# Optimization experiments

Measured on AMD Instinct MI355X. Metric: run time of the kernel, lower is better.

The kernel has to match this reference:

```python
import jax, jax.numpy as jnp
import numpy as np

V, D, H, B, T = 32000, 256, 512, 32, 64


def setup_inputs() -> dict:
    key = jax.random.key(0)
    ks = jax.random.split(key, 8)
    return {
        "word_indices": jax.random.randint(ks[0], (B, T), 0, V),
        "num_words": jax.random.randint(ks[1], (B,), 1, T + 1),
        "encoder_state": jax.random.normal(ks[2], (B, H), jnp.float32),
        # learned params
        "embW": jax.random.uniform(ks[3], (V, D), jnp.float32, -1.0, 1.0),
        "Wg": jax.random.normal(ks[4], (D + H, 2 * H), jnp.float32) * 0.05,  # reset+update gates
        "bg": jnp.ones((2 * H,), jnp.float32),  # TF GRUCell gate bias init = 1.0
        "Wc": jax.random.normal(ks[5], (D + H, H), jnp.float32) * 0.05,      # candidate
        "bc": jnp.zeros((H,), jnp.float32),
        "Wout": jax.random.normal(ks[6], (H, V), jnp.float32) * 0.05,        # Dense(V)
        "bout": jnp.zeros((V,), jnp.float32),
    }


def reference(word_indices, num_words, encoder_state, embW, Wg, bg, Wc, bc, Wout, bout):
    # Embedding lookup: [B, T, D] -> time-major [T, B, D]
    xs = jnp.swapaxes(embW[word_indices], 0, 1)
    # sequence-length mask like tf.nn.static_rnn: [T, B, 1]
    mask = (jnp.arange(T)[:, None] < num_words[None, :])[..., None].astype(xs.dtype)

    def step(h, inp):
        x_t, m_t = inp  # [B, D], [B, 1]
        xh = jnp.concatenate([x_t, h], axis=-1)          # [B, D+H]
        r, u = jnp.split(jax.nn.sigmoid(xh @ Wg + bg), 2, axis=-1)
        c = jnp.tanh(jnp.concatenate([x_t, r * h], axis=-1) @ Wc + bc)
        h_new = u * h + (1.0 - u) * c
        out = h_new * m_t                                 # zero outputs past seq length
        h_next = m_t * h_new + (1.0 - m_t) * h            # carry state past seq length
        return h_next, out

    _, outs = jax.lax.scan(step, encoder_state, (xs, mask))  # outs: [T, B, H]
    logits = jnp.einsum('tbh,hv->btv', outs, Wout) + bout    # [B, T, V]
    return logits
```

## Files before the change

kernel.cpp:

```cpp
#include <hip/hip_runtime.h>
#include <hip/hip_bf16.h>

#define V_ 32000
#define D_ 256
#define H_ 512
#define B_ 32
#define T_ 64
#define NSL 8

typedef __attribute__((ext_vector_type(8))) __bf16 bf16x8;
typedef __attribute__((ext_vector_type(4))) float f32x4;
typedef _Float16 f16x2 __attribute__((ext_vector_type(2)));
typedef unsigned int u32t;
typedef unsigned short u16t;
typedef unsigned long long u64t;

__device__ __forceinline__ u32t pack_h16(float a, float b) {
  union { _Float16 h; unsigned short u; } lo, hi;
  lo.h = (_Float16)a; hi.h = (_Float16)b;
  return (u32t)lo.u | ((u32t)hi.u << 16);
}

__device__ __forceinline__ float f16u_to_f(u16t u) {
  union { _Float16 h; unsigned short u; } x;
  x.u = u;
  return (float)x.h;
}

__device__ __forceinline__ float dot2(u32t w, u32t h, float acc) {
#if __has_builtin(__builtin_amdgcn_fdot2)
  return __builtin_amdgcn_fdot2(__builtin_bit_cast(f16x2, w),
                                __builtin_bit_cast(f16x2, h), acc, false);
#else
  f16x2 a = __builtin_bit_cast(f16x2, w);
  f16x2 b = __builtin_bit_cast(f16x2, h);
  return acc + (float)a.x * (float)b.x + (float)a.y * (float)b.y;
#endif
}

__device__ __forceinline__ void gld_lds16(const void* g, void* l) {
  __builtin_amdgcn_global_load_lds((const __attribute__((address_space(1))) void*)g,
                                   (__attribute__((address_space(3))) void*)l,
                                   16, 0, 0);
}

__device__ __forceinline__ u32t ld_rlx(const u32t* p) {
  return __hip_atomic_load(p, __ATOMIC_RELAXED, __HIP_MEMORY_SCOPE_AGENT);
}
__device__ __forceinline__ void st_rlx(u32t* p, u32t v) {
  __hip_atomic_store(p, v, __ATOMIC_RELAXED, __HIP_MEMORY_SCOPE_AGENT);
}

__global__ __launch_bounds__(256) void k_transpose(const float* __restrict__ Wout,
                                                   __hip_bfloat16* __restrict__ WoutT) {
  __shared__ float tile[64][65];
  int v0 = blockIdx.x * 64;
  int h0 = blockIdx.y * 64;
  int tid = threadIdx.x;
#pragma unroll
  for (int i = 0; i < 16; ++i) {
    int idx = i * 256 + tid;
    int r = idx >> 6;
    int c = idx & 63;
    tile[r][c] = Wout[(size_t)(h0 + r) * V_ + v0 + c];
  }
  __syncthreads();
#pragma unroll
  for (int i = 0; i < 16; ++i) {
    int idx = i * 256 + tid;
    int rv = idx >> 6;
    int ch = idx & 63;
    WoutT[(size_t)(v0 + rv) * H_ + h0 + ch] = __float2bfloat16(tile[ch][rv]);
  }
}

__global__ __launch_bounds__(256) void k_pack_g2(const float* __restrict__ Wg,
                                                 uint4* __restrict__ Wg2) {
  int gid = blockIdx.x * 256 + threadIdx.x;
  int ks = gid & 3;
  int cq = (gid >> 2) & 127;
  int it = (gid >> 9) & 15;
  int s = gid >> 13;
  int j = (cq < 64) ? (s * 64 + cq) : (512 + s * 64 + (cq - 64));
  int k0 = ks * 128 + it * 8;
  uint4 v;
  v.x = pack_h16(Wg[(size_t)(256 + k0 + 0) * 1024 + j], Wg[(size_t)(256 + k0 + 1) * 1024 + j]);
  v.y = pack_h16(Wg[(size_t)(256 + k0 + 2) * 1024 + j], Wg[(size_t)(256 + k0 + 3) * 1024 + j]);
  v.z = pack_h16(Wg[(size_t)(256 + k0 + 4) * 1024 + j], Wg[(size_t)(256 + k0 + 5) * 1024 + j]);
  v.w = pack_h16(Wg[(size_t)(256 + k0 + 6) * 1024 + j], Wg[(size_t)(256 + k0 + 7) * 1024 + j]);
  Wg2[gid] = v;
}
__global__ __launch_bounds__(256) void k_pack_c2(const float* __restrict__ Wc,
                                                 uint4* __restrict__ Wc2) {
  int gid = blockIdx.x * 256 + threadIdx.x;
  int ks8 = gid & 7;
  int cq2 = (gid >> 3) & 63;
  int it = (gid >> 9) & 7;
  int s = gid >> 12;
  int jc = s * 64 + cq2;
  int k0 = ks8 * 64 + it * 8;
  uint4 v;
  v.x = pack_h16(Wc[(size_t)(256 + k0 + 0) * 512 + jc], Wc[(size_t)(256 + k0 + 1) * 512 + jc]);
  v.y = pack_h16(Wc[(size_t)(256 + k0 + 2) * 512 + jc], Wc[(size_t)(256 + k0 + 3) * 512 + jc]);
  v.z = pack_h16(Wc[(size_t)(256 + k0 + 4) * 512 + jc], Wc[(size_t)(256 + k0 + 5) * 512 + jc]);
  v.w = pack_h16(Wc[(size_t)(256 + k0 + 6) * 512 + jc], Wc[(size_t)(256 + k0 + 7) * 512 + jc]);
  Wc2[gid] = v;
}

__global__ __launch_bounds__(256) void k_precompute_g(const int* __restrict__ widx,
                                                      const float* __restrict__ embW,
                                                      const float* __restrict__ Wg,
                                                      const float* __restrict__ bg,
                                                      float* __restrict__ pre_g) {
  __shared__ __align__(16) float x2[D_][8];
  __shared__ int wid[8];
  int tid = threadIdx.x;
  int n0 = blockIdx.x * 8;
  if (tid < 8) wid[tid] = widx[n0 + tid];
  __syncthreads();
#pragma unroll
  for (int i = 0; i < 8; ++i)
    x2[tid][i] = embW[(size_t)wid[i] * D_ + tid];
  __syncthreads();

  int J = blockIdx.y * 256 + tid;
  float bias = bg[J];
  float acc[8];
#pragma unroll
  for (int i = 0; i < 8; ++i) acc[i] = bias;
  for (int d = 0; d < D_; ++d) {
    float4 xa = *(const float4*)&x2[d][0];
    float4 xb = *(const float4*)&x2[d][4];
    float w = Wg[(size_t)d * 1024 + J];
    acc[0] = fmaf(xa.x, w, acc[0]); acc[1] = fmaf(xa.y, w, acc[1]);
    acc[2] = fmaf(xa.z, w, acc[2]); acc[3] = fmaf(xa.w, w, acc[3]);
    acc[4] = fmaf(xb.x, w, acc[4]); acc[5] = fmaf(xb.y, w, acc[5]);
    acc[6] = fmaf(xb.z, w, acc[6]); acc[7] = fmaf(xb.w, w, acc[7]);
  }
#pragma unroll
  for (int i = 0; i < 8; ++i)
    pre_g[(size_t)(n0 + i) * 1024 + J] = acc[i];
}

__global__ __launch_bounds__(256) void k_precompute_c(const int* __restrict__ widx,
                                                      const float* __restrict__ embW,
                                                      const float* __restrict__ Wc,
                                                      const float* __restrict__ bc,
                                                      float* __restrict__ pre_c) {
  __shared__ __align__(16) float x2[D_][8];
  __shared__ int wid[8];
  int tid = threadIdx.x;
  int n0 = blockIdx.x * 8;
  if (tid < 8) wid[tid] = widx[n0 + tid];
  __syncthreads();
#pragma unroll
  for (int i = 0; i < 8; ++i)
    x2[tid][i] = embW[(size_t)wid[i] * D_ + tid];
  __syncthreads();

  int Jc = blockIdx.y * 256 + tid;
  float bias = bc[Jc];
  float acc[8];
#pragma unroll
  for (int i = 0; i < 8; ++i) acc[i] = bias;
  for (int d = 0; d < D_; ++d) {
    float4 xa = *(const float4*)&x2[d][0];
    float4 xb = *(const float4*)&x2[d][4];
    float w = Wc[(size_t)d * 512 + Jc];
    acc[0] = fmaf(xa.x, w, acc[0]); acc[1] = fmaf(xa.y, w, acc[1]);
    acc[2] = fmaf(xa.z, w, acc[2]); acc[3] = fmaf(xa.w, w, acc[3]);
    acc[4] = fmaf(xb.x, w, acc[4]); acc[5] = fmaf(xb.y, w, acc[5]);
    acc[6] = fmaf(xb.z, w, acc[6]); acc[7] = fmaf(xb.w, w, acc[7]);
  }
#pragma unroll
  for (int i = 0; i < 8; ++i)
    pre_c[(size_t)(n0 + i) * 512 + Jc] = acc[i];
}

__global__ __launch_bounds__(256) void k_gru_init(const float* __restrict__ enc,
                                                  u32t* __restrict__ HBT,
                                                  u32t* __restrict__ RHT) {
  int gid = blockIdx.x * 256 + threadIdx.x;
  int b = gid >> 9, k = gid & 511;
  u32t hv = pack_h16(enc[b * H_ + k], 0.f) & 0xffffu;
  st_rlx(&HBT[gid], hv);
  st_rlx(&RHT[gid], 0xFFFF0000u);
}

__global__ __launch_bounds__(512, 2) void k_gru7(const int* __restrict__ num_words,
                                                 const uint4* __restrict__ Wg2,
                                                 const uint4* __restrict__ Wc2,
                                                 const float* __restrict__ pre_g,
                                                 const float* __restrict__ pre_c,
                                                 u32t* __restrict__ RHT,
                                                 u32t* __restrict__ HBT,
                                                 u32t* __restrict__ A32) {
  __shared__ __align__(16) u32t h2_l[256];
  __shared__ __align__(16) u32t rh2_l[256];
  __shared__ float u_l[64];
  int bid = blockIdx.x;
  int b = bid & 31;
  int s = bid >> 5;
  int tid = threadIdx.x;
  int nw = num_words[b];

  int cq = tid >> 2, ks = tid & 3;
  int j1 = (cq < 64) ? (s * 64 + cq) : (512 + s * 64 + (cq - 64));
  int cq2 = tid >> 3, ks8 = tid & 7;
  int jc = s * 64 + cq2;

  uint4 wg[16];
#pragma unroll
  for (int i = 0; i < 16; ++i) {
    int ii = (i + ks) & 15;
    wg[i] = Wg2[(((size_t)s * 16 + ii) * 128 + cq) * 4 + ks];
  }
  uint4 wc[8];
#pragma unroll
  for (int i = 0; i < 8; ++i) {
    int ii = (i + ks8) & 7;
    wc[i] = Wc2[(((size_t)s * 8 + ii) * 64 + cq2) * 8 + ks8];
  }

  u32t* HBp = HBT + (size_t)b * 512;
  u32t* RHp = RHT + (size_t)b * 512;
  bool pub1 = (ks == 0) && (cq < 64);
  bool ulane = (ks == 0) && (cq >= 64);
  bool pub2 = (ks8 == 0);
  bool writer2 = pub2 && ((cq2 & 1) == 0);

  for (int t = 0; t < T_; ++t) {
    float pg = pre_g[((size_t)b * T_ + t) * 1024 + j1];
    float pc = pre_c[((size_t)b * T_ + t) * 512 + jc];

    __syncthreads();
    {
      u32t want = (u32t)t << 16;
      u32t v;
      do { v = ld_rlx(&HBp[tid]); } while ((v & 0xffff0000u) != want);
      ((volatile u16t*)h2_l)[tid] = (u16t)v;
    }
    __syncthreads();

    float a = 0.f;
    const uint4* h4 = (const uint4*)h2_l;
#pragma unroll
    for (int i = 0; i < 16; ++i) {
      int ii = (i + ks) & 15;
      uint4 hv = h4[ks * 16 + ii];
      a = dot2(wg[i].x, hv.x, a);
      a = dot2(wg[i].y, hv.y, a);
      a = dot2(wg[i].z, hv.z, a);
      a = dot2(wg[i].w, hv.w, a);
    }
    a += __shfl_xor(a, 1);
    a += __shfl_xor(a, 2);
    float gate = 1.f / (1.f + __expf(-(a + pg)));
    if (cq < 64) {
      float hh = f16u_to_f(((const u16t*)h2_l)[s * 64 + cq]);
      if (pub1)
        st_rlx(&RHp[s * 64 + cq],
               (pack_h16(gate * hh, 0.f) & 0xffffu) | ((u32t)(t + 1) << 16));
    } else if (ulane) {
      u_l[cq - 64] = gate;
    }

    {
      u32t want = (u32t)(t + 1) << 16;
      u32t v;
      do { v = ld_rlx(&RHp[tid]); } while ((v & 0xffff0000u) != want);
      ((volatile u16t*)rh2_l)[tid] = (u16t)v;
    }
    __syncthreads();

    float a2 = 0.f;
    const uint4* r4 = (const uint4*)rh2_l;
#pragma unroll
    for (int i = 0; i < 8; ++i) {
      int ii = (i + ks8) & 7;
      uint4 rv = r4[ks8 * 8 + ii];
      a2 = dot2(wc[i].x, rv.x, a2);
      a2 = dot2(wc[i].y, rv.y, a2);
      a2 = dot2(wc[i].z, rv.z, a2);
      a2 = dot2(wc[i].w, rv.w, a2);
    }
    a2 += __shfl_xor(a2, 1);
    a2 += __shfl_xor(a2, 2);
    a2 += __shfl_xor(a2, 4);
    float cv = tanhf(a2 + pc);
    float uu = u_l[cq2];
    float hold = f16u_to_f(((const u16t*)h2_l)[jc]);
    float hn = uu * hold + (1.f - uu) * cv;
    bool live = t < nw;
    float hnext = live ? hn : hold;
    if (pub2)
      st_rlx(&HBp[s * 64 + cq2],
             (pack_h16(hnext, 0.f) & 0xffffu) | ((u32t)(t + 1) << 16));
    u32t ma = (u32t)__hip_bfloat16_raw(__float2bfloat16(live ? hn : 0.f)).x;
    u32t oa = (u32t)__shfl_xor((int)ma, 8);
    if (writer2)
      A32[(((size_t)b * T_ + t) * 512 + jc) >> 1] = ma | (oa << 16);
  }
}

__global__ __launch_bounds__(256) void k_proj(const __hip_bfloat16* __restrict__ Ap,
                                              const __hip_bfloat16* __restrict__ BTp,
                                              const float* __restrict__ bout,
                                              float* __restrict__ C) {
  __shared__ char As[128 * 64 * 2];
  __shared__ char Bs[128 * 64 * 2];
  int tid = threadIdx.x;
  int lane = tid & 63;
  int wave = tid >> 6;
  int m0 = blockIdx.x * 128;
  int n0 = blockIdx.y * 128;
  int wm = wave >> 1, wn = wave & 1;
  f32x4 acc[4][4] = {};

  const char* Ab = (const char*)Ap;
  const char* Bb = (const char*)BTp;

  for (int ks = 0; ks < 8; ++ks) {
    int k0 = ks * 64;
    __syncthreads();
#pragma unroll
    for (int inst = 0; inst < 4; ++inst) {
      int o = inst * 4096 + wave * 1024;
      int ol = o + lane * 16;
      int r = ol >> 7;
      int cb = ol & 127;
      gld_lds16(Ab + ((size_t)(m0 + r) * 512 + k0) * 2 + cb, As + o);
      gld_lds16(Bb + ((size_t)(n0 + r) * 512 + k0) * 2 + cb, Bs + o);
    }
    __syncthreads();
#pragma unroll
    for (int kk = 0; kk < 64; kk += 32) {
      bf16x8 af[4], bfr[4];
      int cbyte = kk * 2 + ((lane >> 4) << 4);
#pragma unroll
      for (int mi = 0; mi < 4; ++mi) {
        int row = wm * 64 + mi * 16 + (lane & 15);
        af[mi] = *(const bf16x8*)(As + row * 128 + cbyte);
      }
#pragma unroll
      for (int ni = 0; ni < 4; ++ni) {
        int row = wn * 64 + ni * 16 + (lane & 15);
        bfr[ni] = *(const bf16x8*)(Bs + row * 128 + cbyte);
      }
#pragma unroll
      for (int mi = 0; mi < 4; ++mi)
#pragma unroll
        for (int ni = 0; ni < 4; ++ni)
          acc[mi][ni] = __builtin_amdgcn_mfma_f32_16x16x32_bf16(af[mi], bfr[ni], acc[mi][ni], 0, 0, 0);
    }
  }
#pragma unroll
  for (int ni = 0; ni < 4; ++ni) {
    int col = n0 + wn * 64 + ni * 16 + (lane & 15);
    float bb = bout[col];
#pragma unroll
    for (int mi = 0; mi < 4; ++mi) {
      int rbase = m0 + wm * 64 + mi * 16 + ((lane >> 4) << 2);
#pragma unroll
      for (int rr = 0; rr < 4; ++rr) {
        C[(size_t)(rbase + rr) * V_ + col] = acc[mi][ni][rr] + bb;
      }
    }
  }
}

extern "C" void kernel_launch(void* const* d_in, const int* in_sizes, int n_in,
                              void* d_out, int out_size, void* d_ws, size_t ws_size,
                              hipStream_t stream) {
  const int* widx = (const int*)d_in[0];
  const int* num_words = (const int*)d_in[1];
  const float* enc = (const float*)d_in[2];
  const float* embW = (const float*)d_in[3];
  const float* Wg = (const float*)d_in[4];
  const float* bg = (const float*)d_in[5];
  const float* Wc = (const float*)d_in[6];
  const float* bc = (const float*)d_in[7];
  const float* Wout = (const float*)d_in[8];
  const float* bout = (const float*)d_in[9];
  float* out = (float*)d_out;

  char* ws = (char*)d_ws;
  float* pre_g = (float*)(ws);
  float* pre_c = (float*)(ws + 8388608);
  __hip_bfloat16* A = (__hip_bfloat16*)(ws + 12582912);
  __hip_bfloat16* WoutT = (__hip_bfloat16*)(ws + 14680064);
  uint4* Wg2 = (uint4*)(ws + 47448064);
  uint4* Wc2 = (uint4*)(ws + 48496640);
  u32t* RHT = (u32t*)(ws + 49020928);
  u32t* HBT = (u32t*)(ws + 49086464);

  hipLaunchKernelGGL(k_pack_g2, dim3(256), dim3(256), 0, stream, Wg, Wg2);
  hipLaunchKernelGGL(k_pack_c2, dim3(128), dim3(256), 0, stream, Wc, Wc2);
  hipLaunchKernelGGL(k_transpose, dim3(500, 8), dim3(256), 0, stream, Wout, WoutT);
  hipLaunchKernelGGL(k_precompute_g, dim3(256, 4), dim3(256), 0, stream,
                     widx, embW, Wg, bg, pre_g);
  hipLaunchKernelGGL(k_precompute_c, dim3(256, 2), dim3(256), 0, stream,
                     widx, embW, Wc, bc, pre_c);
  hipLaunchKernelGGL(k_gru_init, dim3(64), dim3(256), 0, stream, enc, HBT, RHT);
  hipLaunchKernelGGL(k_gru7, dim3(32 * NSL), dim3(512), 0, stream,
                     num_words, Wg2, Wc2, pre_g, pre_c, RHT, HBT, (u32t*)A);
  hipLaunchKernelGGL(k_proj, dim3(16, 250), dim3(256), 0, stream, A, WoutT, bout, out);
}
```

Baseline: 390.5 us.

## Fuse GRU recurrence and output projection into one persistent kernel with flag-based streaming

Merges the GRU recurrence kernel and the vocabulary projection GEMM into a single 512-block launch. Blocks 0-255 run the recurrence and publish each hidden-state output with a per-timestep tag. The remaining 256 blocks spin on those tags and start 128-row projection tiles as soon as their timesteps finish, so the large GEMM overlaps the serial recurrence. It also stores pre_c in bf16 and adds an LDS XOR swizzle. The risks are spin-wait traffic, co-residency assumptions for forward progress, a wider tagged A buffer, and smaller M tiles (2x4 MFMA per wave) that reuse B less.

```diff
diff --git a/kernel.cpp b/kernel.cpp
--- a/kernel.cpp
+++ b/kernel.cpp
@@ -146,7 +146,7 @@
                                                       const float* __restrict__ embW,
                                                       const float* __restrict__ Wc,
                                                       const float* __restrict__ bc,
-                                                      float* __restrict__ pre_c) {
+                                                      __hip_bfloat16* __restrict__ pre_c) {
   __shared__ __align__(16) float x2[D_][8];
   __shared__ int wid[8];
   int tid = threadIdx.x;
@@ -174,196 +174,241 @@
   }
 #pragma unroll
   for (int i = 0; i < 8; ++i)
-    pre_c[(size_t)(n0 + i) * 512 + Jc] = acc[i];
+    pre_c[(size_t)(n0 + i) * 512 + Jc] = __float2bfloat16(acc[i]);
 }
 
 __global__ __launch_bounds__(256) void k_gru_init(const float* __restrict__ enc,
                                                   u32t* __restrict__ HBT,
-                                                  u32t* __restrict__ RHT) {
+                                                  u32t* __restrict__ RHT,
+                                                  uint4* __restrict__ AT4) {
   int gid = blockIdx.x * 256 + threadIdx.x;
   int b = gid >> 9, k = gid & 511;
   u32t hv = pack_h16(enc[b * H_ + k], 0.f) & 0xffffu;
   st_rlx(&HBT[gid], hv);
   st_rlx(&RHT[gid], 0xFFFF0000u);
-}
-
-__global__ __launch_bounds__(512, 2) void k_gru7(const int* __restrict__ num_words,
-                                                 const uint4* __restrict__ Wg2,
-                                                 const uint4* __restrict__ Wc2,
-                                                 const float* __restrict__ pre_g,
-                                                 const float* __restrict__ pre_c,
-                                                 u32t* __restrict__ RHT,
-                                                 u32t* __restrict__ HBT,
-                                                 u32t* __restrict__ A32) {
+  uint4 z = {0u, 0u, 0u, 0u};
+#pragma unroll
+  for (int i = 0; i < 16; ++i)
+    AT4[(size_t)gid * 16 + i] = z;
+}
+
+__global__ __launch_bounds__(512, 4) void k_fused(const int* __restrict__ num_words,
+                                                  const uint4* __restrict__ Wg2,
+                                                  const uint4* __restrict__ Wc2,
+                                                  const float* __restrict__ pre_g,
+                                                  const __hip_bfloat16* __restrict__ pre_c,
+                                                  u32t* __restrict__ RHT,
+                                                  u32t* __restrict__ HBT,
+                                                  u32t* __restrict__ AT,
+                                                  const __hip_bfloat16* __restrict__ BT,
+                                                  const float* __restrict__ bout,
+                                                  float* __restrict__ C) {
   __shared__ __align__(16) u32t h2_l[256];
   __shared__ __align__(16) u32t rh2_l[256];
   __shared__ float u_l[64];
+  __shared__ __align__(16) char As[128 * 128];
+  __shared__ __align__(16) char Bs[128 * 128];
   int bid = blockIdx.x;
-  int b = bid & 31;
-  int s = bid >> 5;
   int tid = threadIdx.x;
-  int nw = num_words[b];
-
-  int cq = tid >> 2, ks = tid & 3;
-  int j1 = (cq < 64) ? (s * 64 + cq) : (512 + s * 64 + (cq - 64));
-  int cq2 = tid >> 3, ks8 = tid & 7;
-  int jc = s * 64 + cq2;
-
-  uint4 wg[16];
-#pragma unroll
-  for (int i = 0; i < 16; ++i) {
-    int ii = (i + ks) & 15;
-    wg[i] = Wg2[(((size_t)s * 16 + ii) * 128 + cq) * 4 + ks];
-  }
-  uint4 wc[8];
-#pragma unroll
-  for (int i = 0; i < 8; ++i) {
-    int ii = (i + ks8) & 7;
-    wc[i] = Wc2[(((size_t)s * 8 + ii) * 64 + cq2) * 8 + ks8];
-  }
-
-  u32t* HBp = HBT + (size_t)b * 512;
-  u32t* RHp = RHT + (size_t)b * 512;
-  bool pub1 = (ks == 0) && (cq < 64);
-  bool ulane = (ks == 0) && (cq >= 64);
-  bool pub2 = (ks8 == 0);
-  bool writer2 = pub2 && ((cq2 & 1) == 0);
-
-  for (int t = 0; t < T_; ++t) {
-    float pg = pre_g[((size_t)b * T_ + t) * 1024 + j1];
-    float pc = pre_c[((size_t)b * T_ + t) * 512 + jc];
-
-    __syncthreads();
-    {
-      u32t want = (u32t)t << 16;
-      u32t v;
-      do { v = ld_rlx(&HBp[tid]); } while ((v & 0xffff0000u) != want);
-      ((volatile u16t*)h2_l)[tid] = (u16t)v;
-    }
-    __syncthreads();
-
-    float a = 0.f;
-    const uint4* h4 = (const uint4*)h2_l;
+
+  if (bid < 256) {
+    int b = bid & 31;
+    int s = bid >> 5;
+    int nw = num_words[b];
+
+    int cq = tid >> 2, ks = tid & 3;
+    int j1 = (cq < 64) ? (s * 64 + cq) : (512 + s * 64 + (cq - 64));
+    int cq2 = tid >> 3, ks8 = tid & 7;
+    int jc = s * 64 + cq2;
+
+    uint4 wg[16];
 #pragma unroll
     for (int i = 0; i < 16; ++i) {
       int ii = (i + ks) & 15;
-      uint4 hv = h4[ks * 16 + ii];
-      a = dot2(wg[i].x, hv.x, a);
-      a = dot2(wg[i].y, hv.y, a);
-      a = dot2(wg[i].z, hv.z, a);
-      a = dot2(wg[i].w, hv.w, a);
+      wg[i] = Wg2[(((size_t)s * 16 + ii) * 128 + cq) * 4 + ks];
     }
-    a += __shfl_xor(a, 1);
-    a += __shfl_xor(a, 2);
-    float gate = 1.f / (1.f + __expf(-(a + pg)));
-    if (cq < 64) {
-      float hh = f16u_to_f(((const u16t*)h2_l)[s * 64 + cq]);
-      if (pub1)
-        st_rlx(&RHp[s * 64 + cq],
-               (pack_h16(gate * hh, 0.f) & 0xffffu) | ((u32t)(t + 1) << 16));
-    } else if (ulane) {
-      u_l[cq - 64] = gate;
-    }
-
-    {
-      u32t want = (u32t)(t + 1) << 16;
-      u32t v;
-      do { v = ld_rlx(&RHp[tid]); } while ((v & 0xffff0000u) != want);
-      ((volatile u16t*)rh2_l)[tid] = (u16t)v;
-    }
-    __syncthreads();
-
-    float a2 = 0.f;
-    const uint4* r4 = (const uint4*)rh2_l;
+    uint4 wc[8];
 #pragma unroll
     for (int i = 0; i < 8; ++i) {
       int ii = (i + ks8) & 7;
-      uint4 rv = r4[ks8 * 8 + ii];
-      a2 = dot2(wc[i].x, rv.x, a2);
-      a2 = dot2(wc[i].y, rv.y, a2);
-      a2 = dot2(wc[i].z, rv.z, a2);
-      a2 = dot2(wc[i].w, rv.w, a2);
+      wc[i] = Wc2[(((size_t)s * 8 + ii) * 64 + cq2) * 8 + ks8];
     }
-    a2 += __shfl_xor(a2, 1);
-    a2 += __shfl_xor(a2, 2);
-    a2 += __shfl_xor(a2, 4);
-    float cv = tanhf(a2 + pc);
-    float uu = u_l[cq2];
-    float hold = f16u_to_f(((const u16t*)h2_l)[jc]);
-    float hn = uu * hold + (1.f - uu) * cv;
-    bool live = t < nw;
-    float hnext = live ? hn : hold;
-    if (pub2)
-      st_rlx(&HBp[s * 64 + cq2],
-             (pack_h16(hnext, 0.f) & 0xffffu) | ((u32t)(t + 1) << 16));
-    u32t ma = (u32t)__hip_bfloat16_raw(__float2bfloat16(live ? hn : 0.f)).x;
-    u32t oa = (u32t)__shfl_xor((int)ma, 8);
-    if (writer2)
-      A32[(((size_t)b * T_ + t) * 512 + jc) >> 1] = ma | (oa << 16);
-  }
-}
-
-__global__ __launch_bounds__(256) void k_proj(const __hip_bfloat16* __restrict__ Ap,
-                                              const __hip_bfloat16* __restrict__ BTp,
-                                              const float* __restrict__ bout,
-                                              float* __restrict__ C) {
-  __shared__ char As[128 * 64 * 2];
-  __shared__ char Bs[128 * 64 * 2];
-  int tid = threadIdx.x;
-  int lane = tid & 63;
-  int wave = tid >> 6;
-  int m0 = blockIdx.x * 128;
-  int n0 = blockIdx.y * 128;
-  int wm = wave >> 1, wn = wave & 1;
-  f32x4 acc[4][4] = {};
-
-  const char* Ab = (const char*)Ap;
-  const char* Bb = (const char*)BTp;
-
-  for (int ks = 0; ks < 8; ++ks) {
-    int k0 = ks * 64;
-    __syncthreads();
-#pragma unroll
-    for (int inst = 0; inst < 4; ++inst) {
-      int o = inst * 4096 + wave * 1024;
-      int ol = o + lane * 16;
-      int r = ol >> 7;
-      int cb = ol & 127;
-      gld_lds16(Ab + ((size_t)(m0 + r) * 512 + k0) * 2 + cb, As + o);
-      gld_lds16(Bb + ((size_t)(n0 + r) * 512 + k0) * 2 + cb, Bs + o);
+
+    u32t* HBp = HBT + (size_t)b * 512;
+    u32t* RHp = RHT + (size_t)b * 512;
+    bool pub1 = (ks == 0) && (cq < 64);
+    bool ulane = (ks == 0) && (cq >= 64);
+    bool pub2 = (ks8 == 0);
+
+    for (int t = 0; t < T_; ++t) {
+      float pg = pre_g[((size_t)b * T_ + t) * 1024 + j1];
+      float pc = __bfloat162float(pre_c[((size_t)b * T_ + t) * 512 + jc]);
+
+      __syncthreads();
+      {
+        u32t want = (u32t)t << 16;
+        u32t v;
+        do { v = ld_rlx(&HBp[tid]); } while ((v & 0xffff0000u) != want);
+        ((volatile u16t*)h2_l)[tid] = (u16t)v;
+      }
+      __syncthreads();
+
+      float a = 0.f;
+      const uint4* h4 = (const uint4*)h2_l;
+#pragma unroll
+      for (int i = 0; i < 16; ++i) {
+        int ii = (i + ks) & 15;
+        uint4 hv = h4[ks * 16 + ii];
+        a = dot2(wg[i].x, hv.x, a);
+        a = dot2(wg[i].y, hv.y, a);
+        a = dot2(wg[i].z, hv.z, a);
+        a = dot2(wg[i].w, hv.w, a);
+      }
+      a += __shfl_xor(a, 1);
+      a += __shfl_xor(a, 2);
+      float gate = 1.f / (1.f + __expf(-(a + pg)));
+      if (cq < 64) {
+        float hh = f16u_to_f(((const u16t*)h2_l)[s * 64 + cq]);
+        if (pub1)
+          st_rlx(&RHp[s * 64 + cq],
+                 (pack_h16(gate * hh, 0.f) & 0xffffu) | ((u32t)(t + 1) << 16));
+      } else if (ulane) {
+        u_l[cq - 64] = gate;
+      }
+
+      {
+        u32t want = (u32t)(t + 1) << 16;
+        u32t v;
+        do { v = ld_rlx(&RHp[tid]); } while ((v & 0xffff0000u) != want);
+        ((volatile u16t*)rh2_l)[tid] = (u16t)v;
+      }
+      __syncthreads();
+
+      float a2 = 0.f;
+      const uint4* r4 = (const uint4*)rh2_l;
+#pragma unroll
+      for (int i = 0; i < 8; ++i) {
+        int ii = (i + ks8) & 7;
+        uint4 rv = r4[ks8 * 8 + ii];
+        a2 = dot2(wc[i].x, rv.x, a2);
+        a2 = dot2(wc[i].y, rv.y, a2);
+        a2 = dot2(wc[i].z, rv.z, a2);
+        a2 = dot2(wc[i].w, rv.w, a2);
+      }
+      a2 += __shfl_xor(a2, 1);
+      a2 += __shfl_xor(a2, 2);
+      a2 += __shfl_xor(a2, 4);
+      float cv = tanhf(a2 + pc);
+      float uu = u_l[cq2];
+      float hold = f16u_to_f(((const u16t*)h2_l)[jc]);
+      float hn = uu * hold + (1.f - uu) * cv;
+      bool live = t < nw;
+      float hnext = live ? hn : hold;
+      if (pub2) {
+        st_rlx(&HBp[s * 64 + cq2],
+               (pack_h16(hnext, 0.f) & 0xffffu) | ((u32t)(t + 1) << 16));
+        u32t av = (u32t)__hip_bfloat16_raw(__float2bfloat16(live ? hn : 0.f)).x;
+        st_rlx(&AT[((size_t)(t * 32 + b)) * 512 + jc], av | ((u32t)(t + 1) << 16));
+      }
     }
-    __syncthreads();
-#pragma unroll
-    for (int kk = 0; kk < 64; kk += 32) {
-      bf16x8 af[4], bfr[4];
-      int cbyte = kk * 2 + ((lane >> 4) << 4);
-#pragma unroll
-      for (int mi = 0; mi < 4; ++mi) {
-        int row = wm * 64 + mi * 16 + (lane & 15);
-        af[mi] = *(const bf16x8*)(As + row * 128 + cbyte);
-      }
-#pragma unroll
-      for (int ni = 0; ni < 4; ++ni) {
-        int row = wn * 64 + ni * 16 + (lane & 15);
-        bfr[ni] = *(const bf16x8*)(Bs + row * 128 + cbyte);
-      }
-#pragma unroll
-      for (int mi = 0; mi < 4; ++mi)
-#pragma unroll
-        for (int ni = 0; ni < 4; ++ni)
-          acc[mi][ni] = __builtin_amdgcn_mfma_f32_16x16x32_bf16(af[mi], bfr[ni], acc[mi][ni], 0, 0, 0);
-    }
-  }
-#pragma unroll
-  for (int ni = 0; ni < 4; ++ni) {
-    int col = n0 + wn * 64 + ni * 16 + (lane & 15);
-    float bb = bout[col];
-#pragma unroll
-    for (int mi = 0; mi < 4; ++mi) {
-      int rbase = m0 + wm * 64 + mi * 16 + ((lane >> 4) << 2);
-#pragma unroll
-      for (int rr = 0; rr < 4; ++rr) {
-        C[(size_t)(rbase + rr) * V_ + col] = acc[mi][ni][rr] + bb;
+  } else {
+    int vid = bid - 256;
+    int lane = tid & 63;
+    int wave = tid >> 6;
+    int wm = wave >> 1;
+    int wn = wave & 1;
+    int arow = tid >> 2;
+    int akq = (tid & 3) << 4;
+    int aswz = (arow & 7) << 4;
+    const char* Bb = (const char*)BT;
+
+    for (int g4 = 0; g4 < 4; ++g4) {
+#pragma unroll 1
+      for (int j4 = 0; j4 < 4; ++j4) {
+        int tau = g4 * 1024 + vid * 4 + j4;
+        if (tau >= 4000) continue;
+        int m = tau / 250;
+        int n = tau - m * 250;
+        u32t want = ((u32t)((m << 2) + (arow >> 5) + 1)) << 16;
+        const u32t* Arow = AT + ((size_t)(m * 128 + arow)) * 512 + akq;
+
+        f32x4 acc[2][4];
+#pragma unroll
+        for (int mi = 0; mi < 2; ++mi)
+#pragma unroll
+          for (int ni = 0; ni < 4; ++ni)
+            acc[mi][ni] = (f32x4){0.f, 0.f, 0.f, 0.f};
+
+        for (int ksx = 0; ksx < 8; ++ksx) {
+          __syncthreads();
+          const u32t* Asrc = Arow + ksx * 64;
+#pragma unroll
+          for (int half = 0; half < 2; ++half) {
+            u32t v[8];
+            bool ok;
+            do {
+              ok = true;
+#pragma unroll
+              for (int e = 0; e < 8; ++e) v[e] = ld_rlx(&Asrc[half * 8 + e]);
+#pragma unroll
+              for (int e = 0; e < 8; ++e) ok &= ((v[e] & 0xffff0000u) == want);
+              if (!ok) __builtin_amdgcn_s_sleep(1);
+            } while (!ok);
+            uint4 p;
+            p.x = (v[0] & 0xffffu) | (v[1] << 16);
+            p.y = (v[2] & 0xffffu) | (v[3] << 16);
+            p.z = (v[4] & 0xffffu) | (v[5] << 16);
+            p.w = (v[6] & 0xffffu) | (v[7] << 16);
+            int kb = (akq + half * 8) * 2;
+            *(uint4*)(As + arow * 128 + (kb ^ aswz)) = p;
+          }
+#pragma unroll
+          for (int inst = 0; inst < 2; ++inst) {
+            int o = inst * 8192 + wave * 1024;
+            int ol = o + lane * 16;
+            int r = ol >> 7;
+            int cb = ol & 127;
+            int cbs = cb ^ ((r & 7) << 4);
+            gld_lds16(Bb + ((size_t)(n * 128 + r) * 512 + ksx * 64) * 2 + cbs, Bs + o);
+          }
+          __syncthreads();
+#pragma unroll
+          for (int kk = 0; kk < 64; kk += 32) {
+            int cbyte = kk * 2 + ((lane >> 4) << 4);
+            bf16x8 af[2], bfr[4];
+#pragma unroll
+            for (int mi = 0; mi < 2; ++mi) {
+              int row = wm * 32 + mi * 16 + (lane & 15);
+              af[mi] = *(const bf16x8*)(As + row * 128 + (cbyte ^ ((row & 7) << 4)));
+            }
+#pragma unroll
+            for (int ni = 0; ni < 4; ++ni) {
+              int row = wn * 64 + ni * 16 + (lane & 15);
+              bfr[ni] = *(const bf16x8*)(Bs + row * 128 + (cbyte ^ ((row & 7) << 4)));
+            }
+#pragma unroll
+            for (int mi = 0; mi < 2; ++mi)
+#pragma unroll
+              for (int ni = 0; ni < 4; ++ni)
+                acc[mi][ni] = __builtin_amdgcn_mfma_f32_16x16x32_bf16(af[mi], bfr[ni], acc[mi][ni], 0, 0, 0);
+          }
+        }
+#pragma unroll
+        for (int ni = 0; ni < 4; ++ni) {
+          int col = n * 128 + wn * 64 + ni * 16 + (lane & 15);
+          float bb = bout[col];
+#pragma unroll
+          for (int mi = 0; mi < 2; ++mi) {
+            int r0 = m * 128 + wm * 32 + mi * 16 + ((lane >> 4) << 2);
+#pragma unroll
+            for (int rr = 0; rr < 4; ++rr) {
+              int r = r0 + rr;
+              int tt = r >> 5;
+              int bb2 = r & 31;
+              C[((size_t)(bb2 * T_ + tt)) * V_ + col] = acc[mi][ni][rr] + bb;
+            }
+          }
+        }
       }
     }
   }
@@ -386,8 +431,8 @@
 
   char* ws = (char*)d_ws;
   float* pre_g = (float*)(ws);
-  float* pre_c = (float*)(ws + 8388608);
-  __hip_bfloat16* A = (__hip_bfloat16*)(ws + 12582912);
+  __hip_bfloat16* pre_c = (__hip_bfloat16*)(ws + 8388608);
+  u32t* AT = (u32t*)(ws + 10485760);
   __hip_bfloat16* WoutT = (__hip_bfloat16*)(ws + 14680064);
   uint4* Wg2 = (uint4*)(ws + 47448064);
   uint4* Wc2 = (uint4*)(ws + 48496640);
@@ -401,8 +446,9 @@
                      widx, embW, Wg, bg, pre_g);
   hipLaunchKernelGGL(k_precompute_c, dim3(256, 2), dim3(256), 0, stream,
                      widx, embW, Wc, bc, pre_c);
-  hipLaunchKernelGGL(k_gru_init, dim3(64), dim3(256), 0, stream, enc, HBT, RHT);
-  hipLaunchKernelGGL(k_gru7, dim3(32 * NSL), dim3(512), 0, stream,
-                     num_words, Wg2, Wc2, pre_g, pre_c, RHT, HBT, (u32t*)A);
-  hipLaunchKernelGGL(k_proj, dim3(16, 250), dim3(256), 0, stream, A, WoutT, bout, out);
-}
+  hipLaunchKernelGGL(k_gru_init, dim3(64), dim3(256), 0, stream, enc, HBT, RHT,
+                     (uint4*)AT);
+  hipLaunchKernelGGL(k_fused, dim3(512), dim3(512), 0, stream,
+                     num_words, Wg2, Wc2, pre_g, pre_c, RHT, HBT, AT,
+                     WoutT, bout, out);
+}
```

Result: slower. 1.442 ms (+269.2%).
